# Optimization experiments

Measured on AMD Instinct MI355X. Metric: run time of the kernel, lower is better.

## Reference

```python
import jax, jax.numpy as jnp
import numpy as np

N, E, DIN, DOUT, EDIM = 100000, 1000000, 64, 64, 64


def _xavier(k, shape, gain=1.0):
    fan_out, fan_in = shape
    a = gain * np.sqrt(6.0 / (fan_in + fan_out))
    return jax.random.uniform(k, shape, jnp.float32, -a, a)


def setup_inputs() -> dict:
    key = jax.random.key(0)
    ks = jax.random.split(key, 16)
    relu_gain = float(np.sqrt(2.0))  # nn.init.calculate_gain('relu')
    return {
        "nfeats": jax.random.normal(ks[0], (N, DIN), jnp.float32),
        "efeats": jax.random.normal(ks[1], (E, EDIM), jnp.float32),
        "src": jax.random.randint(ks[2], (E,), 0, N),
        "dst": jax.random.randint(ks[3], (E,), 0, N),
        "e_perm": jax.random.permutation(ks[4], E),
        # layer 0 params (torch Linear layout: [out, in])
        "Wmsg0": _xavier(ks[5], (DOUT, DIN + EDIM)),
        "bmsg0": jnp.zeros((DOUT,), jnp.float32),
        "Wapply0": _xavier(ks[6], (DOUT, DIN + DOUT), relu_gain),
        "bapply0": jnp.zeros((DOUT,), jnp.float32),
        # layer 1 params
        "Wmsg1": _xavier(ks[7], (DOUT, DOUT + EDIM)),
        "bmsg1": jnp.zeros((DOUT,), jnp.float32),
        "Wapply1": _xavier(ks[8], (DOUT, DOUT + DOUT), relu_gain),
        "bapply1": jnp.zeros((DOUT,), jnp.float32),
    }


def _sage_layer(h, ef, src, dst, Wmsg, bmsg, Wap, bap, n_nodes):
    # message: W_msg(cat(src_h, e_h)) per edge  -> [E, dout]
    m = jnp.concatenate([h[src], ef], axis=1) @ Wmsg.T + bmsg
    # mean-reduce messages onto destination nodes
    s = jax.ops.segment_sum(m, dst, num_segments=n_nodes)
    cnt = jax.ops.segment_sum(jnp.ones((dst.shape[0],), m.dtype), dst, num_segments=n_nodes)
    h_neigh = s / jnp.maximum(cnt, 1.0)[:, None]  # zero-in-degree nodes -> 0
    return jax.nn.relu(jnp.concatenate([h, h_neigh], axis=1) @ Wap.T + bap)


def _bce_with_logits(x, target):
    # mean(log(1+exp(x)) - x*target), numerically stable via logaddexp
    return jnp.mean(jnp.logaddexp(0.0, x) - x * target)


def reference(nfeats, efeats, src, dst, e_perm,
              Wmsg0, bmsg0, Wapply0, bapply0,
              Wmsg1, bmsg1, Wapply1, bapply1):
    n_nodes = nfeats.shape[0]

    def encode(ef):
        h = _sage_layer(nfeats, ef, src, dst, Wmsg0, bmsg0, Wapply0, bapply0, n_nodes)
        h = _sage_layer(h, ef, src, dst, Wmsg1, bmsg1, Wapply1, bapply1, n_nodes)
        return h

    positive = encode(efeats)
    negative = encode(efeats[e_perm])  # corrupted view: permuted edge features
    P_LABEL, N_LABEL = 1.0, 0.0  # DGI p / n targets
    return _bce_with_logits(positive, P_LABEL) + _bce_with_logits(negative, N_LABEL)
```

## Files before the change

### kernel.cpp

```cpp
#include <hip/hip_runtime.h>
#include <math.h>

#define NN 100000
#define NE 1000000
#define D  64
#define NB_SCAN 391


__global__ __launch_bounds__(256) void k_hist(
    const int* __restrict__ dst, int* __restrict__ counts, int* __restrict__ rank)
{
    int e = blockIdx.x * 256 + threadIdx.x;
    if (e >= NE) return;
    rank[e] = atomicAdd(&counts[dst[e]], 1);
}

__global__ __launch_bounds__(256) void k_scan1(
    const int* __restrict__ counts, int* __restrict__ row_start, int* __restrict__ bsum)
{
    __shared__ int s[256];
    int t = threadIdx.x;
    int i = blockIdx.x * 256 + t;
    int v = (i < NN) ? counts[i] : 0;
    s[t] = v; __syncthreads();
#pragma unroll
    for (int off = 1; off < 256; off <<= 1) {
        int add = (t >= off) ? s[t - off] : 0;
        __syncthreads();
        s[t] += add;
        __syncthreads();
    }
    if (i < NN) row_start[i] = s[t] - v;
    if (t == 255) bsum[blockIdx.x] = s[255];
}

__global__ __launch_bounds__(512) void k_scan2(
    const int* __restrict__ bsum, int* __restrict__ boff, int* __restrict__ row_start)
{
    __shared__ int s[512];
    int t = threadIdx.x;
    int v = (t < NB_SCAN) ? bsum[t] : 0;
    s[t] = v; __syncthreads();
#pragma unroll
    for (int off = 1; off < 512; off <<= 1) {
        int add = (t >= off) ? s[t - off] : 0;
        __syncthreads();
        s[t] += add;
        __syncthreads();
    }
    if (t < NB_SCAN) boff[t] = s[t] - v;
    if (t == 0) row_start[NN] = NE;
}

__global__ __launch_bounds__(256) void k_scan3(
    int* __restrict__ row_start, const int* __restrict__ boff)
{
    int i = blockIdx.x * 256 + threadIdx.x;
    if (i < NN) row_start[i] += boff[i >> 8];
}

__global__ __launch_bounds__(256) void k_scatter(
    const int* __restrict__ dst, const int* __restrict__ src,
    const int* __restrict__ perm, const int* __restrict__ rank,
    const int* __restrict__ row_start, int4* __restrict__ sorted)
{
    int e = blockIdx.x * 256 + threadIdx.x;
    if (e >= NE) return;
    int pos = row_start[dst[e]] + rank[e];
    sorted[pos] = make_int4(src[e], e, perm[e], 0);
}


__global__ __launch_bounds__(256) void pull_pass1(
    const int4* __restrict__ sorted, const int* __restrict__ row_start,
    const float* __restrict__ nfeats, const float* __restrict__ efeats,
    float* __restrict__ hsum0, float* __restrict__ efsP, float* __restrict__ efsN)
{
    int gt = blockIdx.x * 256 + threadIdx.x;
    int w = gt >> 6, lane = gt & 63;
    if (w >= NN) return;
    int es = lane >> 4, c4 = (lane & 15) << 2;
    int beg = row_start[w], end = row_start[w + 1];

    float an0 = 0.f, an1 = 0.f, an2 = 0.f, an3 = 0.f;
    float ap0 = 0.f, ap1 = 0.f, ap2 = 0.f, ap3 = 0.f;
    float ag0 = 0.f, ag1 = 0.f, ag2 = 0.f, ag3 = 0.f;
#pragma unroll 1
    for (int i = beg + es; i < end; i += 4) {
        int4 q = sorted[i];
        float4 n  = *(const float4*)(nfeats + (size_t)q.x * D + c4);
        float4 ep = *(const float4*)(efeats + (size_t)q.y * D + c4);
        float4 en = *(const float4*)(efeats + (size_t)q.z * D + c4);
        an0 += n.x;  an1 += n.y;  an2 += n.z;  an3 += n.w;
        ap0 += ep.x; ap1 += ep.y; ap2 += ep.z; ap3 += ep.w;
        ag0 += en.x; ag1 += en.y; ag2 += en.z; ag3 += en.w;
    }
#pragma unroll
    for (int off = 16; off <= 32; off <<= 1) {
        an0 += __shfl_xor(an0, off, 64); an1 += __shfl_xor(an1, off, 64);
        an2 += __shfl_xor(an2, off, 64); an3 += __shfl_xor(an3, off, 64);
        ap0 += __shfl_xor(ap0, off, 64); ap1 += __shfl_xor(ap1, off, 64);
        ap2 += __shfl_xor(ap2, off, 64); ap3 += __shfl_xor(ap3, off, 64);
        ag0 += __shfl_xor(ag0, off, 64); ag1 += __shfl_xor(ag1, off, 64);
        ag2 += __shfl_xor(ag2, off, 64); ag3 += __shfl_xor(ag3, off, 64);
    }
    if (lane < 16) {
        *(float4*)(hsum0 + (size_t)w * D + c4) = make_float4(an0, an1, an2, an3);
        *(float4*)(efsP  + (size_t)w * D + c4) = make_float4(ap0, ap1, ap2, ap3);
        *(float4*)(efsN  + (size_t)w * D + c4) = make_float4(ag0, ag1, ag2, ag3);
    }
}

__global__ __launch_bounds__(256) void pull_h(
    const int4* __restrict__ sorted, const int* __restrict__ row_start,
    const float* __restrict__ h, float* __restrict__ hsum)
{
    int gt = blockIdx.x * 256 + threadIdx.x;
    int w = gt >> 6, lane = gt & 63;
    if (w >= NN) return;
    int es = lane >> 4, c4 = (lane & 15) << 2;
    int beg = row_start[w], end = row_start[w + 1];

    float a0 = 0.f, a1 = 0.f, a2 = 0.f, a3 = 0.f;
#pragma unroll 2
    for (int i = beg + es; i < end; i += 4) {
        int4 q = sorted[i];
        float4 v = *(const float4*)(h + (size_t)q.x * D + c4);
        a0 += v.x; a1 += v.y; a2 += v.z; a3 += v.w;
    }
#pragma unroll
    for (int off = 16; off <= 32; off <<= 1) {
        a0 += __shfl_xor(a0, off, 64); a1 += __shfl_xor(a1, off, 64);
        a2 += __shfl_xor(a2, off, 64); a3 += __shfl_xor(a3, off, 64);
    }
    if (lane < 16)
        *(float4*)(hsum + (size_t)w * D + c4) = make_float4(a0, a1, a2, a3);
}

__global__ __launch_bounds__(256, 4) void fused_layer(
    const float* __restrict__ Hsum, const float* __restrict__ Esum,
    const float* __restrict__ Hprev, const int* __restrict__ counts,
    const float* __restrict__ Wmsg, const float* __restrict__ bmsg,
    const float* __restrict__ Wap, const float* __restrict__ bap,
    float* __restrict__ Hout, int do_loss, int is_neg, float* __restrict__ loss_out)
{
    __shared__ __align__(16) float As[64][68];
    __shared__ __align__(16) float Bs[128][68];
    int tid = threadIdx.x;
    int block0 = blockIdx.x * 64;
    int tx = tid & 15, ty = tid >> 4;
    int tx4 = tx << 2;

#pragma unroll 1
    for (int i = 0; i < 32; ++i) {
        int idx = i * 256 + tid;
        Bs[idx & 127][idx >> 7] = Wmsg[idx];
    }

    float acc[4][4] = {};
#pragma unroll
    for (int half = 0; half < 2; ++half) {
        const float* Asrc = half ? Esum : Hsum;
        __syncthreads();
#pragma unroll
        for (int g = 0; g < 4; ++g) {
            int idx = g * 256 + tid;
            int node = idx >> 4, c = (idx & 15) << 2;
            int gn = block0 + node;
            float4 v = make_float4(0.f, 0.f, 0.f, 0.f);
            if (gn < NN) v = *(const float4*)(Asrc + (size_t)gn * D + c);
            *(float4*)&As[node][c] = v;
        }
        __syncthreads();
        int hb = half * 64;
#pragma unroll 1
        for (int k0 = 0; k0 < 64; k0 += 4) {
            float a[4][4];
#pragma unroll
            for (int i = 0; i < 4; ++i)
                *(float4*)&a[i][0] = *(const float4*)&As[ty + 16 * i][k0];
#pragma unroll
            for (int kk = 0; kk < 4; ++kk) {
                float4 b = *(const float4*)&Bs[hb + k0 + kk][tx4];
#pragma unroll
                for (int i = 0; i < 4; ++i) {
                    acc[i][0] += a[i][kk] * b.x;
                    acc[i][1] += a[i][kk] * b.y;
                    acc[i][2] += a[i][kk] * b.z;
                    acc[i][3] += a[i][kk] * b.w;
                }
            }
        }
    }

    float bm[4];
#pragma unroll
    for (int j = 0; j < 4; ++j) bm[j] = bmsg[tx4 + j];
    float msg[4][4];
#pragma unroll
    for (int i = 0; i < 4; ++i) {
        int gn = block0 + ty + 16 * i;
        float c = (gn < NN) ? (float)counts[gn] : 0.f;
        float inv = 1.0f / fmaxf(c, 1.0f);
#pragma unroll
        for (int j = 0; j < 4; ++j) msg[i][j] = (acc[i][j] + c * bm[j]) * inv;
    }

    __syncthreads();
#pragma unroll 1
    for (int i = 0; i < 32; ++i) {
        int idx = i * 256 + tid;
        Bs[idx & 127][idx >> 7] = Wap[idx];
    }
#pragma unroll
    for (int i = 0; i < 4; ++i)
        *(float4*)&As[ty + 16 * i][tx4] = make_float4(msg[i][0], msg[i][1], msg[i][2], msg[i][3]);
    __syncthreads();

    float acc2[4][4] = {};
#pragma unroll 1
    for (int k0 = 0; k0 < 64; k0 += 4) {
        float a[4][4];
#pragma unroll
        for (int i = 0; i < 4; ++i)
            *(float4*)&a[i][0] = *(const float4*)&As[ty + 16 * i][k0];
#pragma unroll
        for (int kk = 0; kk < 4; ++kk) {
            float4 b = *(const float4*)&Bs[64 + k0 + kk][tx4];
#pragma unroll
            for (int i = 0; i < 4; ++i) {
                acc2[i][0] += a[i][kk] * b.x;
                acc2[i][1] += a[i][kk] * b.y;
                acc2[i][2] += a[i][kk] * b.z;
                acc2[i][3] += a[i][kk] * b.w;
            }
        }
    }
    __syncthreads();
#pragma unroll
    for (int g = 0; g < 4; ++g) {
        int idx = g * 256 + tid;
        int node = idx >> 4, c = (idx & 15) << 2;
        int gn = block0 + node;
        float4 v = make_float4(0.f, 0.f, 0.f, 0.f);
        if (gn < NN) v = *(const float4*)(Hprev + (size_t)gn * D + c);
        *(float4*)&As[node][c] = v;
    }
    __syncthreads();
#pragma unroll 1
    for (int k0 = 0; k0 < 64; k0 += 4) {
        float a[4][4];
#pragma unroll
        for (int i = 0; i < 4; ++i)
            *(float4*)&a[i][0] = *(const float4*)&As[ty + 16 * i][k0];
#pragma unroll
        for (int kk = 0; kk < 4; ++kk) {
            float4 b = *(const float4*)&Bs[k0 + kk][tx4];
#pragma unroll
            for (int i = 0; i < 4; ++i) {
                acc2[i][0] += a[i][kk] * b.x;
                acc2[i][1] += a[i][kk] * b.y;
                acc2[i][2] += a[i][kk] * b.z;
                acc2[i][3] += a[i][kk] * b.w;
            }
        }
    }

    float ba[4];
#pragma unroll
    for (int j = 0; j < 4; ++j) ba[j] = bap[tx4 + j];
    if (!do_loss) {
#pragma unroll
        for (int i = 0; i < 4; ++i) {
            int gn = block0 + ty + 16 * i;
            if (gn >= NN) continue;
#pragma unroll
            for (int j = 0; j < 4; ++j)
                Hout[(size_t)gn * D + tx4 + j] = fmaxf(acc2[i][j] + ba[j], 0.f);
        }
    } else {
        float lsum = 0.f;
#pragma unroll
        for (int i = 0; i < 4; ++i) {
            int gn = block0 + ty + 16 * i;
            if (gn >= NN) continue;
#pragma unroll
            for (int j = 0; j < 4; ++j) {
                float x = fmaxf(acc2[i][j] + ba[j], 0.f);
                float l = log1pf(expf(-x));
                if (is_neg) l += x;
                lsum += l;
            }
        }
#pragma unroll
        for (int off = 32; off; off >>= 1) lsum += __shfl_down(lsum, off, 64);
        if ((tid & 63) == 0)
            unsafeAtomicAdd(loss_out, lsum * (1.0f / 6400000.0f));
    }
}

extern "C" void kernel_launch(void* const* d_in, const int* in_sizes, int n_in,
                              void* d_out, int out_size, void* d_ws, size_t ws_size,
                              hipStream_t stream) {
    (void)in_sizes; (void)n_in; (void)out_size; (void)ws_size;
    const float* nfeats = (const float*)d_in[0];
    const float* efeats = (const float*)d_in[1];
    const int*   src    = (const int*)d_in[2];
    const int*   dst    = (const int*)d_in[3];
    const int*   perm   = (const int*)d_in[4];
    const float* Wmsg0  = (const float*)d_in[5];
    const float* bmsg0  = (const float*)d_in[6];
    const float* Wap0   = (const float*)d_in[7];
    const float* bap0   = (const float*)d_in[8];
    const float* Wmsg1  = (const float*)d_in[9];
    const float* bmsg1  = (const float*)d_in[10];
    const float* Wap1   = (const float*)d_in[11];
    const float* bap1   = (const float*)d_in[12];
    float* out = (float*)d_out;

    const size_t NV = (size_t)NN * D;
    char* p = (char*)d_ws;
    int4* sorted   = (int4*)p;               p += (size_t)NE * 16;
    int*  rank     = (int*)p;                p += (size_t)NE * 4;
    int*  counts   = (int*)p;                p += ((NN + 15) & ~15) * 4;
    int*  rowst    = (int*)p;                p += ((NN + 16) & ~15) * 4;
    int*  bsum     = (int*)p;                p += 512 * 4;
    int*  boff     = (int*)p;                p += 512 * 4;
    float* efsP    = (float*)p;              p += NV * 4;
    float* efsN    = (float*)p;              p += NV * 4;
    float* hsum0   = (float*)p;              p += NV * 4;
    float* h1      = (float*)p;              p += NV * 4;
    float* hsum1   = (float*)p;              p += NV * 4;

    const int EGb = (NE + 255) / 256;
    const int PGb = ((size_t)NN * 64 + 255) / 256;
    const int NG  = (NN + 63) / 64;

    hipMemsetAsync(counts, 0, (size_t)NN * 4, stream);
    hipMemsetAsync(d_out, 0, 4, stream);

    k_hist<<<EGb, 256, 0, stream>>>(dst, counts, rank);
    k_scan1<<<NB_SCAN, 256, 0, stream>>>(counts, rowst, bsum);
    k_scan2<<<1, 512, 0, stream>>>(bsum, boff, rowst);
    k_scan3<<<NB_SCAN, 256, 0, stream>>>(rowst, boff);
    k_scatter<<<EGb, 256, 0, stream>>>(dst, src, perm, rank, rowst, sorted);

    pull_pass1<<<PGb, 256, 0, stream>>>(sorted, rowst, nfeats, efeats, hsum0, efsP, efsN);

    fused_layer<<<NG, 256, 0, stream>>>(hsum0, efsP, nfeats, counts,
                                        Wmsg0, bmsg0, Wap0, bap0, h1, 0, 0, nullptr);
    pull_h<<<PGb, 256, 0, stream>>>(sorted, rowst, h1, hsum1);
    fused_layer<<<NG, 256, 0, stream>>>(hsum1, efsP, h1, counts,
                                        Wmsg1, bmsg1, Wap1, bap1, nullptr, 1, 0, out);

    fused_layer<<<NG, 256, 0, stream>>>(hsum0, efsN, nfeats, counts,
                                        Wmsg0, bmsg0, Wap0, bap0, h1, 0, 0, nullptr);
    pull_h<<<PGb, 256, 0, stream>>>(sorted, rowst, h1, hsum1);
    fused_layer<<<NG, 256, 0, stream>>>(hsum1, efsN, h1, counts,
                                        Wmsg1, bmsg1, Wap1, bap1, nullptr, 1, 1, out);
}
```

Before: 1.029 ms.

## Fuse positive and negative second-layer gathers and add compact sorted source index

Reorders the schedule so both views' first layers run before a single merged gather kernel, which pulls neighbour features for the positive and negative views in one pass over the CSR. That pass reads a new compact int array of sorted sources instead of the 16-byte int4 records. The pass-1 and gather loops also prefetch the next edge index one iteration ahead. The cost is extra workspace for separate per-view buffers and an extra write in the scatter.

```diff
diff --git a/kernel.cpp b/kernel.cpp
--- a/kernel.cpp
+++ b/kernel.cpp
@@ -62,12 +62,15 @@
 __global__ __launch_bounds__(256) void k_scatter(
     const int* __restrict__ dst, const int* __restrict__ src,
     const int* __restrict__ perm, const int* __restrict__ rank,
-    const int* __restrict__ row_start, int4* __restrict__ sorted)
+    const int* __restrict__ row_start, int4* __restrict__ sorted,
+    int* __restrict__ srcS)
 {
     int e = blockIdx.x * 256 + threadIdx.x;
     if (e >= NE) return;
+    int s = src[e];
     int pos = row_start[dst[e]] + rank[e];
-    sorted[pos] = make_int4(src[e], e, perm[e], 0);
+    sorted[pos] = make_int4(s, e, perm[e], 0);
+    srcS[pos] = s;
 }
 
 
@@ -85,15 +88,19 @@
     float an0 = 0.f, an1 = 0.f, an2 = 0.f, an3 = 0.f;
     float ap0 = 0.f, ap1 = 0.f, ap2 = 0.f, ap3 = 0.f;
     float ag0 = 0.f, ag1 = 0.f, ag2 = 0.f, ag3 = 0.f;
-#pragma unroll 1
-    for (int i = beg + es; i < end; i += 4) {
-        int4 q = sorted[i];
+    int i = beg + es;
+    int4 q = (i < end) ? sorted[i] : make_int4(0, 0, 0, 0);
+#pragma unroll 1
+    for (; i < end; i += 4) {
+        int inext = i + 4;
+        int4 qn = (inext < end) ? sorted[inext] : make_int4(0, 0, 0, 0);
         float4 n  = *(const float4*)(nfeats + (size_t)q.x * D + c4);
         float4 ep = *(const float4*)(efeats + (size_t)q.y * D + c4);
         float4 en = *(const float4*)(efeats + (size_t)q.z * D + c4);
         an0 += n.x;  an1 += n.y;  an2 += n.z;  an3 += n.w;
         ap0 += ep.x; ap1 += ep.y; ap2 += ep.z; ap3 += ep.w;
         ag0 += en.x; ag1 += en.y; ag2 += en.z; ag3 += en.w;
+        q = qn;
     }
 #pragma unroll
     for (int off = 16; off <= 32; off <<= 1) {
@@ -111,9 +118,10 @@
     }
 }
 
-__global__ __launch_bounds__(256) void pull_h(
-    const int4* __restrict__ sorted, const int* __restrict__ row_start,
-    const float* __restrict__ h, float* __restrict__ hsum)
+__global__ __launch_bounds__(256) void pull_h2(
+    const int* __restrict__ srcS, const int* __restrict__ row_start,
+    const float* __restrict__ hP, const float* __restrict__ hN,
+    float* __restrict__ hsumP, float* __restrict__ hsumN)
 {
     int gt = blockIdx.x * 256 + threadIdx.x;
     int w = gt >> 6, lane = gt & 63;
@@ -121,20 +129,31 @@
     int es = lane >> 4, c4 = (lane & 15) << 2;
     int beg = row_start[w], end = row_start[w + 1];
 
-    float a0 = 0.f, a1 = 0.f, a2 = 0.f, a3 = 0.f;
-#pragma unroll 2
-    for (int i = beg + es; i < end; i += 4) {
-        int4 q = sorted[i];
-        float4 v = *(const float4*)(h + (size_t)q.x * D + c4);
-        a0 += v.x; a1 += v.y; a2 += v.z; a3 += v.w;
+    float p0 = 0.f, p1 = 0.f, p2 = 0.f, p3 = 0.f;
+    float n0 = 0.f, n1 = 0.f, n2 = 0.f, n3 = 0.f;
+    int i = beg + es;
+    int s = (i < end) ? srcS[i] : 0;
+#pragma unroll 1
+    for (; i < end; i += 4) {
+        int inext = i + 4;
+        int sn = (inext < end) ? srcS[inext] : 0;
+        float4 vP = *(const float4*)(hP + (size_t)s * D + c4);
+        float4 vN = *(const float4*)(hN + (size_t)s * D + c4);
+        p0 += vP.x; p1 += vP.y; p2 += vP.z; p3 += vP.w;
+        n0 += vN.x; n1 += vN.y; n2 += vN.z; n3 += vN.w;
+        s = sn;
     }
 #pragma unroll
     for (int off = 16; off <= 32; off <<= 1) {
-        a0 += __shfl_xor(a0, off, 64); a1 += __shfl_xor(a1, off, 64);
-        a2 += __shfl_xor(a2, off, 64); a3 += __shfl_xor(a3, off, 64);
-    }
-    if (lane < 16)
-        *(float4*)(hsum + (size_t)w * D + c4) = make_float4(a0, a1, a2, a3);
+        p0 += __shfl_xor(p0, off, 64); p1 += __shfl_xor(p1, off, 64);
+        p2 += __shfl_xor(p2, off, 64); p3 += __shfl_xor(p3, off, 64);
+        n0 += __shfl_xor(n0, off, 64); n1 += __shfl_xor(n1, off, 64);
+        n2 += __shfl_xor(n2, off, 64); n3 += __shfl_xor(n3, off, 64);
+    }
+    if (lane < 16) {
+        *(float4*)(hsumP + (size_t)w * D + c4) = make_float4(p0, p1, p2, p3);
+        *(float4*)(hsumN + (size_t)w * D + c4) = make_float4(n0, n1, n2, n3);
+    }
 }
 
 __global__ __launch_bounds__(256, 4) void fused_layer(
@@ -321,6 +340,7 @@
     const size_t NV = (size_t)NN * D;
     char* p = (char*)d_ws;
     int4* sorted   = (int4*)p;               p += (size_t)NE * 16;
+    int*  srcS     = (int*)p;                p += (size_t)NE * 4;
     int*  rank     = (int*)p;                p += (size_t)NE * 4;
     int*  counts   = (int*)p;                p += ((NN + 15) & ~15) * 4;
     int*  rowst    = (int*)p;                p += ((NN + 16) & ~15) * 4;
@@ -329,8 +349,10 @@
     float* efsP    = (float*)p;              p += NV * 4;
     float* efsN    = (float*)p;              p += NV * 4;
     float* hsum0   = (float*)p;              p += NV * 4;
-    float* h1      = (float*)p;              p += NV * 4;
-    float* hsum1   = (float*)p;              p += NV * 4;
+    float* h1P     = (float*)p;              p += NV * 4;
+    float* h1N     = (float*)p;              p += NV * 4;
+    float* hsum1P  = (float*)p;              p += NV * 4;
+    float* hsum1N  = (float*)p;              p += NV * 4;
 
     const int EGb = (NE + 255) / 256;
     const int PGb = ((size_t)NN * 64 + 255) / 256;
@@ -343,19 +365,19 @@
     k_scan1<<<NB_SCAN, 256, 0, stream>>>(counts, rowst, bsum);
     k_scan2<<<1, 512, 0, stream>>>(bsum, boff, rowst);
     k_scan3<<<NB_SCAN, 256, 0, stream>>>(rowst, boff);
-    k_scatter<<<EGb, 256, 0, stream>>>(dst, src, perm, rank, rowst, sorted);
+    k_scatter<<<EGb, 256, 0, stream>>>(dst, src, perm, rank, rowst, sorted, srcS);
 
     pull_pass1<<<PGb, 256, 0, stream>>>(sorted, rowst, nfeats, efeats, hsum0, efsP, efsN);
 
     fused_layer<<<NG, 256, 0, stream>>>(hsum0, efsP, nfeats, counts,
-                                        Wmsg0, bmsg0, Wap0, bap0, h1, 0, 0, nullptr);
-    pull_h<<<PGb, 256, 0, stream>>>(sorted, rowst, h1, hsum1);
-    fused_layer<<<NG, 256, 0, stream>>>(hsum1, efsP, h1, counts,
+                                        Wmsg0, bmsg0, Wap0, bap0, h1P, 0, 0, nullptr);
+    fused_layer<<<NG, 256, 0, stream>>>(hsum0, efsN, nfeats, counts,
+                                        Wmsg0, bmsg0, Wap0, bap0, h1N, 0, 0, nullptr);
+
+    pull_h2<<<PGb, 256, 0, stream>>>(srcS, rowst, h1P, h1N, hsum1P, hsum1N);
+
+    fused_layer<<<NG, 256, 0, stream>>>(hsum1P, efsP, h1P, counts,
                                         Wmsg1, bmsg1, Wap1, bap1, nullptr, 1, 0, out);
-
-    fused_layer<<<NG, 256, 0, stream>>>(hsum0, efsN, nfeats, counts,
-                                        Wmsg0, bmsg0, Wap0, bap0, h1, 0, 0, nullptr);
-    pull_h<<<PGb, 256, 0, stream>>>(sorted, rowst, h1, hsum1);
-    fused_layer<<<NG, 256, 0, stream>>>(hsum1, efsN, h1, counts,
+    fused_layer<<<NG, 256, 0, stream>>>(hsum1N, efsN, h1N, counts,
                                         Wmsg1, bmsg1, Wap1, bap1, nullptr, 1, 1, out);
 }
```

Result: no change. 1.041 ms (+1.2%).
